# Optimization experiments

Hardware: AMD Instinct MI355X
Metric: run time of the kernel (lower is better)

Reference implementation:

```python
import jax, jax.numpy as jnp
import numpy as np

B, C, H, W = 8, 128, 128, 128
P = 32768
STRIDE = (1.0, 1.0)
TOKEN_FORMAT = 'xy'


def setup_inputs() -> dict:
    key = jax.random.key(0)
    k1, k2 = jax.random.split(key)
    # points mostly in-range [0, W-1], with some out-of-bounds to exercise masking
    tk_codes = jax.random.uniform(k1, (B, P, 2), dtype=jnp.float32, minval=-2.0, maxval=130.0)
    feat_grid = jax.random.normal(k2, (B, C, H, W), dtype=jnp.float32)
    return {"tk_codes": tk_codes, "feat_grid": feat_grid}


def reference(tk_codes, feat_grid):
    b, c, h, w = feat_grid.shape
    pts = tk_codes[..., :2].astype(jnp.float32)
    pts = pts / jnp.array([STRIDE[0], STRIDE[1]], dtype=jnp.float32)
    lead_shape = pts.shape[:-1]
    pts = pts.reshape(b, -1, 2)  # [B, P, 2]
    x, y = pts[..., 0], pts[..., 1]

    # zero weight for out-of-bounds points (matches sequential mask assignments)
    in_bounds = (x >= 0) & (y >= 0) & (x <= w - 1) & (y <= h - 1)  # [B, P]

    fx, cx = jnp.floor(x), jnp.ceil(x)
    fy, cy = jnp.floor(y), jnp.ceil(y)
    # 4 corners in order (floor,floor), (floor,ceil), (ceil,floor), (ceil,ceil) on (x, y)
    corner_x = jnp.stack([fx, fx, cx, cx], axis=2)  # [B, P, 4]
    corner_y = jnp.stack([fy, cy, fy, cy], axis=2)

    gx = jnp.fmod(corner_x.astype(jnp.int32), w)
    gy = jnp.fmod(corner_y.astype(jnp.int32), h)
    gx = jnp.maximum(gx, 0)
    gy = jnp.maximum(gy, 0)

    # inverse-distance weights to the (wrapped/clamped) integer corners
    dx = pts[:, :, None, 0] - gx.astype(jnp.float32)
    dy = pts[:, :, None, 1] - gy.astype(jnp.float32)
    dist_inv = 1.0 / (jnp.sqrt(dx * dx + dy * dy) + 1e-10)  # [B, P, 4]
    wgt = in_bounds[..., None].astype(jnp.float32) * dist_inv
    denom = jnp.sum(wgt, axis=-1, keepdims=True)
    denom = jnp.where(denom == 0.0, 1.0, denom)
    wgt = wgt / denom

    if TOKEN_FORMAT == 'xy':
        flat_idx = gy * w + gx  # [B, P, 4]
    else:  # 'hw'
        flat_idx = gx * w + gy

    fg = jnp.transpose(feat_grid, (0, 2, 3, 1)).reshape(b, h * w, c)  # [B, HW, C]
    vals = jnp.take_along_axis(fg, flat_idx.reshape(b, -1, 1), axis=1)  # [B, P*4, C]
    vals = vals.reshape(b, -1, 4, c)
    out = jnp.sum(vals * wgt[..., None], axis=2)  # [B, P, C]
    return out.reshape(*lead_shape, c)
```

## Files before the change

kernel.cpp:

```cpp
#include <hip/hip_runtime.h>

#define BB 8
#define CC 128
#define HH 128
#define WW 128
#define PP 32768
#define HWW (HH * WW)

typedef float v4f __attribute__((ext_vector_type(4)));

__device__ inline unsigned short cvt_bf16_rne(float f) {
    unsigned int u = __float_as_uint(f);
    unsigned int r = (u + 0x7fffu + ((u >> 16) & 1u)) >> 16;
    return (unsigned short)r;
}

__global__ __launch_bounds__(256) void transpose_bf16_kernel(
    const float* __restrict__ in,
    unsigned short* __restrict__ out)
{
    __shared__ float tile[64][132];
    const int blk = blockIdx.x;
    const int b = blk & 7;
    const int chunk = blk >> 3;
    const int sBase = chunk * 64;
    const int tid = threadIdx.x;

    const float* inb = in + (size_t)b * CC * HWW;
    unsigned short* outb = out + (size_t)b * HWW * CC;

    const int tx = tid & 15;
    const int c0 = tid >> 4;
    const int xw = (tx & 3) << 3;
#pragma unroll
    for (int i = 0; i < 8; ++i) {
        const int c = c0 + 16 * i;
        const v4f v = __builtin_nontemporal_load(
            (const v4f*)(inb + (size_t)c * HWW + sBase + 4 * tx));
        const int xc = c ^ xw;
#pragma unroll
        for (int j = 0; j < 4; ++j)
            tile[4 * tx + j][xc] = v[j];
    }
    __syncthreads();

    const int cx = tid & 15;
    const int s0 = tid >> 4;
#pragma unroll
    for (int i = 0; i < 4; ++i) {
        const int s = s0 + 16 * i;
        const int xv = ((s >> 2) & 3) << 3;
        const int base = (8 * cx) ^ xv;
        const v4f a = *(const v4f*)&tile[s][base];
        const v4f d = *(const v4f*)&tile[s][base + 4];
        uint4 h;
        h.x = (unsigned)cvt_bf16_rne(a[0]) | ((unsigned)cvt_bf16_rne(a[1]) << 16);
        h.y = (unsigned)cvt_bf16_rne(a[2]) | ((unsigned)cvt_bf16_rne(a[3]) << 16);
        h.z = (unsigned)cvt_bf16_rne(d[0]) | ((unsigned)cvt_bf16_rne(d[1]) << 16);
        h.w = (unsigned)cvt_bf16_rne(d[2]) | ((unsigned)cvt_bf16_rne(d[3]) << 16);
        *(uint4*)(outb + (size_t)(sBase + s) * CC + 8 * cx) = h;
    }
}

__device__ inline void compute_corners(float x, float y,
                                       int gx[4], int gy[4], float wgt[4])
{
    const bool inb = (x >= 0.f) && (y >= 0.f) &&
                     (x <= (float)(WW - 1)) && (y <= (float)(HH - 1));
    const float fx = floorf(x), cx = ceilf(x);
    const float fy = floorf(y), cy = ceilf(y);
    const float corx[4] = {fx, fx, cx, cx};
    const float cory[4] = {fy, cy, fy, cy};
    float denom = 0.f;
#pragma unroll
    for (int k = 0; k < 4; ++k) {
        int gxi = ((int)corx[k]) % WW;
        int gyi = ((int)cory[k]) % HH;
        if (gxi < 0) gxi = 0;
        if (gyi < 0) gyi = 0;
        const float dx = x - (float)gxi;
        const float dy = y - (float)gyi;
        const float dinv = __builtin_amdgcn_rcpf(sqrtf(dx * dx + dy * dy) + 1e-10f);
        const float w = inb ? dinv : 0.f;
        gx[k] = gxi;
        gy[k] = gyi;
        wgt[k] = w;
        denom += w;
    }
    const float rden = (denom == 0.f) ? 1.f : __builtin_amdgcn_rcpf(denom);
#pragma unroll
    for (int k = 0; k < 4; ++k) wgt[k] *= rden;
}

__global__ __launch_bounds__(256) void gather_fused_kernel(
    const float* __restrict__ tk,
    const unsigned short* __restrict__ grid,
    float* __restrict__ out)
{
    const int blk = blockIdx.x;
    const int b = blk & 7;
    const int inner = blk >> 3;
    const int grp = (int)threadIdx.x >> 4;
    const int l = (int)threadIdx.x & 15;

    const int p = b * PP + inner * 16 + grp;
    const float2 xy = ((const float2*)tk)[p];

    int gx[4], gy[4];
    float w[4];
    compute_corners(xy.x, xy.y, gx, gy, w);

    const unsigned short* gb = grid + (size_t)b * HWW * CC;
    v4f acc0 = {0.f, 0.f, 0.f, 0.f};
    v4f acc1 = {0.f, 0.f, 0.f, 0.f};
#pragma unroll
    for (int k = 0; k < 4; ++k) {
        const int id = gy[k] * WW + gx[k];
        const uint4 u = *(const uint4*)(gb + (size_t)id * CC + 8 * l);
        v4f v0, v1;
        v0[0] = __uint_as_float(u.x << 16);
        v0[1] = __uint_as_float(u.x & 0xffff0000u);
        v0[2] = __uint_as_float(u.y << 16);
        v0[3] = __uint_as_float(u.y & 0xffff0000u);
        v1[0] = __uint_as_float(u.z << 16);
        v1[1] = __uint_as_float(u.z & 0xffff0000u);
        v1[2] = __uint_as_float(u.w << 16);
        v1[3] = __uint_as_float(u.w & 0xffff0000u);
        acc0 += w[k] * v0;
        acc1 += w[k] * v1;
    }
    v4f* ob = (v4f*)(out + (size_t)p * CC + 8 * l);
    __builtin_nontemporal_store(acc0, ob);
    __builtin_nontemporal_store(acc1, ob + 1);
}

__global__ __launch_bounds__(256) void gather_nchw_kernel(
    const float* __restrict__ tk,
    const float* __restrict__ grid,
    float* __restrict__ out)
{
    const int wave = (int)((blockIdx.x * blockDim.x + threadIdx.x) >> 6);
    const int lane = threadIdx.x & 63;
    if (wave >= BB * PP) return;
    const int b = wave >> 15;

    const float2 xy = ((const float2*)tk)[wave];
    int gx[4], gy[4];
    float wgt[4];
    compute_corners(xy.x, xy.y, gx, gy, wgt);

    const float* gb = grid + (size_t)b * CC * HWW;
    const int c0 = lane * 2;
    float a0 = 0.f, a1 = 0.f;
#pragma unroll
    for (int k = 0; k < 4; ++k) {
        const int sidx = gy[k] * WW + gx[k];
        a0 += wgt[k] * gb[(size_t)c0 * HWW + sidx];
        a1 += wgt[k] * gb[(size_t)(c0 + 1) * HWW + sidx];
    }
    ((float2*)out)[(size_t)wave * (CC / 2) + lane] = make_float2(a0, a1);
}

extern "C" void kernel_launch(void* const* d_in, const int* in_sizes, int n_in,
                              void* d_out, int out_size, void* d_ws, size_t ws_size,
                              hipStream_t stream) {
    const float* tk = (const float*)d_in[0];
    const float* fg = (const float*)d_in[1];
    float* out = (float*)d_out;

    const size_t gridBytes = (size_t)BB * HWW * CC * 2;

    if (ws_size >= gridBytes) {
        unsigned short* gbf = (unsigned short*)d_ws;

        transpose_bf16_kernel<<<(BB * HWW) / 64, 256, 0, stream>>>(fg, gbf);
        gather_fused_kernel<<<(BB * PP) / 16, 256, 0, stream>>>(tk, gbf, out);
    } else {
        const int blocks = (BB * PP * 64) / 256;
        gather_nchw_kernel<<<blocks, 256, 0, stream>>>(tk, fg, out);
    }
}
```

Measured before the change: 207.8 us.

## Split corner-weight computation into separate kernel and narrow gather per-lane width

Corner indices and normalized weights move out of the gather kernel into a new per-point kernel that writes packed ushort4 indices and float4 weights to workspace. The gather kernel then reads these precomputed values, so the 16 lanes that shared a point no longer each recompute the same corners. The gather layout also changes from 16 lanes per point with 16-byte loads to 32 lanes per point with 8-byte loads, giving 8 points per block. The cost is an extra kernel launch, more workspace and an extra round trip through global memory for indices and weights.

```diff
diff --git a/kernel.cpp b/kernel.cpp
--- a/kernel.cpp
+++ b/kernel.cpp
@@ -92,46 +92,61 @@
     for (int k = 0; k < 4; ++k) wgt[k] *= rden;
 }
 
-__global__ __launch_bounds__(256) void gather_fused_kernel(
+__global__ __launch_bounds__(256) void weights_kernel(
     const float* __restrict__ tk,
+    ushort4* __restrict__ idx_out,
+    float4* __restrict__ wgt_out)
+{
+    const int p = blockIdx.x * 256 + (int)threadIdx.x;
+    const float2 xy = ((const float2*)tk)[p];
+
+    int gx[4], gy[4];
+    float wgt[4];
+    compute_corners(xy.x, xy.y, gx, gy, wgt);
+
+    ushort4 id;
+    id.x = (unsigned short)(gy[0] * WW + gx[0]);
+    id.y = (unsigned short)(gy[1] * WW + gx[1]);
+    id.z = (unsigned short)(gy[2] * WW + gx[2]);
+    id.w = (unsigned short)(gy[3] * WW + gx[3]);
+    idx_out[p] = id;
+    wgt_out[p] = make_float4(wgt[0], wgt[1], wgt[2], wgt[3]);
+}
+
+__global__ __launch_bounds__(256) void gather_bf16_kernel(
     const unsigned short* __restrict__ grid,
+    const ushort4* __restrict__ idxs,
+    const float4* __restrict__ wgts,
     float* __restrict__ out)
 {
     const int blk = blockIdx.x;
     const int b = blk & 7;
     const int inner = blk >> 3;
-    const int grp = (int)threadIdx.x >> 4;
-    const int l = (int)threadIdx.x & 15;
-
-    const int p = b * PP + inner * 16 + grp;
-    const float2 xy = ((const float2*)tk)[p];
-
-    int gx[4], gy[4];
-    float w[4];
-    compute_corners(xy.x, xy.y, gx, gy, w);
+    const int wave = (int)threadIdx.x >> 6;
+    const int half = ((int)threadIdx.x >> 5) & 1;
+    const int sub = (int)threadIdx.x & 31;
+
+    const int p = b * PP + inner * 8 + wave * 2 + half;
+
+    const ushort4 id = idxs[p];
+    const float4 w = wgts[p];
 
     const unsigned short* gb = grid + (size_t)b * HWW * CC;
-    v4f acc0 = {0.f, 0.f, 0.f, 0.f};
-    v4f acc1 = {0.f, 0.f, 0.f, 0.f};
+    const int idk[4] = {id.x, id.y, id.z, id.w};
+    const float wk[4] = {w.x, w.y, w.z, w.w};
+
+    v4f acc = {0.f, 0.f, 0.f, 0.f};
 #pragma unroll
     for (int k = 0; k < 4; ++k) {
-        const int id = gy[k] * WW + gx[k];
-        const uint4 u = *(const uint4*)(gb + (size_t)id * CC + 8 * l);
-        v4f v0, v1;
-        v0[0] = __uint_as_float(u.x << 16);
-        v0[1] = __uint_as_float(u.x & 0xffff0000u);
-        v0[2] = __uint_as_float(u.y << 16);
-        v0[3] = __uint_as_float(u.y & 0xffff0000u);
-        v1[0] = __uint_as_float(u.z << 16);
-        v1[1] = __uint_as_float(u.z & 0xffff0000u);
-        v1[2] = __uint_as_float(u.w << 16);
-        v1[3] = __uint_as_float(u.w & 0xffff0000u);
-        acc0 += w[k] * v0;
-        acc1 += w[k] * v1;
-    }
-    v4f* ob = (v4f*)(out + (size_t)p * CC + 8 * l);
-    __builtin_nontemporal_store(acc0, ob);
-    __builtin_nontemporal_store(acc1, ob + 1);
+        const uint2 u = *(const uint2*)(gb + (size_t)idk[k] * CC + 4 * sub);
+        v4f v;
+        v[0] = __uint_as_float(u.x << 16);
+        v[1] = __uint_as_float(u.x & 0xffff0000u);
+        v[2] = __uint_as_float(u.y << 16);
+        v[3] = __uint_as_float(u.y & 0xffff0000u);
+        acc += wk[k] * v;
+    }
+    __builtin_nontemporal_store(acc, (v4f*)out + (size_t)p * (CC / 4) + sub);
 }
 
 __global__ __launch_bounds__(256) void gather_nchw_kernel(
@@ -169,12 +184,18 @@
     float* out = (float*)d_out;
 
     const size_t gridBytes = (size_t)BB * HWW * CC * 2;
-
-    if (ws_size >= gridBytes) {
+    const size_t idxBytes  = (size_t)BB * PP * sizeof(ushort4);
+    const size_t wgtBytes  = (size_t)BB * PP * sizeof(float4);
+    const size_t need = gridBytes + idxBytes + wgtBytes;
+
+    if (ws_size >= need) {
         unsigned short* gbf = (unsigned short*)d_ws;
+        ushort4* idxs = (ushort4*)((char*)d_ws + gridBytes);
+        float4*  wgts = (float4*)((char*)d_ws + gridBytes + idxBytes);
 
         transpose_bf16_kernel<<<(BB * HWW) / 64, 256, 0, stream>>>(fg, gbf);
-        gather_fused_kernel<<<(BB * PP) / 16, 256, 0, stream>>>(tk, gbf, out);
+        weights_kernel<<<(BB * PP) / 256, 256, 0, stream>>>(tk, idxs, wgts);
+        gather_bf16_kernel<<<(BB * PP) / 8, 256, 0, stream>>>(gbf, idxs, wgts, out);
     } else {
         const int blocks = (BB * PP * 64) / 256;
         gather_nchw_kernel<<<blocks, 256, 0, stream>>>(tk, fg, out);
```

Measured after the change: 199.4 us. -4.0%, faster.
